# Performance work log

Measured on AMD Instinct MI355X. Metric: run time of the kernel, lower is better.

The kernel has to match this reference:

```python
import jax, jax.numpy as jnp
import numpy as np

B, S, H = 8, 2048, 256
MAX_SEQ = 2048


def get_rotary_matrix(context_window, embedding_dim):
    # Faithful to the llama-from-scratch construction (note the (i-1) quirk):
    # theta_i = 10000 ** (-2*(i-1)/d) for i in [0, d/2)
    half = embedding_dim // 2
    i = jnp.arange(half, dtype=jnp.float32)
    theta = jnp.power(10000.0, -2.0 * (i - 1.0) / embedding_dim)  # [half]
    pos = jnp.arange(context_window, dtype=jnp.float32)  # [S]
    ang = pos[:, None] * theta[None, :]  # [S, half]
    c, s = jnp.cos(ang), jnp.sin(ang)
    R = jnp.zeros((context_window, embedding_dim, embedding_dim), dtype=jnp.float32)
    idx = jnp.arange(half)
    R = R.at[:, 2 * idx, 2 * idx].set(c)
    R = R.at[:, 2 * idx, 2 * idx + 1].set(-s)
    R = R.at[:, 2 * idx + 1, 2 * idx].set(s)
    R = R.at[:, 2 * idx + 1, 2 * idx + 1].set(c)
    return R


def setup_inputs() -> dict:
    key = jax.random.key(0)
    kx, kq, kk, kv = jax.random.split(key, 4)
    scale = 1.0 / np.sqrt(H)
    x = jax.random.normal(kx, (B, S, H), dtype=jnp.float32)
    wq = jax.random.uniform(kq, (H, H), dtype=jnp.float32, minval=-scale, maxval=scale)
    wk = jax.random.uniform(kk, (H, H), dtype=jnp.float32, minval=-scale, maxval=scale)
    wv = jax.random.uniform(kv, (H, H), dtype=jnp.float32, minval=-scale, maxval=scale)
    r = get_rotary_matrix(MAX_SEQ, H)
    return {"x": x, "wq": wq, "wk": wk, "wv": wv, "r": r}


def reference(x, wq, wk, wv, r):
    b, s, h = x.shape
    # nn.Linear(bias=False): y = x @ W.T
    q = jnp.einsum("bsh,oh->bso", x, wq)
    k = jnp.einsum("bsh,oh->bso", x, wk)
    v = jnp.einsum("bsh,oh->bso", x, wv)
    # per-position dense rotary rotation: qr[b,s,:] = q[b,s,:] @ r[s]
    rs = r[:s]
    qr = jnp.einsum("bsh,shk->bsk", q, rs)
    kr = jnp.einsum("bsh,shk->bsk", k, rs)
    attn = jnp.einsum("bqh,bkh->bqk", qr, kr) * (h ** -0.5)  # [B,S,S]
    causal = jnp.tril(jnp.ones((s, s), dtype=bool))
    attn = jnp.where(causal[None, :, :], attn, -jnp.inf)
    attn = jax.nn.softmax(attn, axis=-1)
    out = jnp.einsum("bqk,bkh->bqh", attn, v)
    return out
```

## Files before the change

### kernel.cpp

```cpp
#include <hip/hip_runtime.h>


typedef __bf16 bf16x8 __attribute__((ext_vector_type(8)));
typedef float  f32x4  __attribute__((ext_vector_type(4)));
typedef unsigned short u16x4 __attribute__((ext_vector_type(4)));

#define LOG2E 1.44269504088896340736f
#define LOG2_10000 13.287712379549449f

__device__ __forceinline__ unsigned short f2bf(float f) {
    union { __bf16 h; unsigned short u; } cv;
    cv.h = (__bf16)f;
    return cv.u;
}

__device__ __forceinline__ void gl_lds16(const unsigned short* g, unsigned short* lds) {
    __builtin_amdgcn_global_load_lds(
        (const __attribute__((address_space(1))) unsigned int*)g,
        (__attribute__((address_space(3))) unsigned int*)lds, 16, 0, 0);
}

#define BARRIER_MEMFENCE() asm volatile("s_barrier" ::: "memory")
#define WAITVM(n) asm volatile("s_waitcnt vmcnt(" #n ")" ::: "memory")

__global__ __launch_bounds__(256) void prep(
    const float* __restrict__ wq, const float* __restrict__ wk,
    const float* __restrict__ wv,
    float2* __restrict__ cs, unsigned short* __restrict__ wb) {
    int bid = blockIdx.x;
    if (bid < 1024) {
        int id = bid * 256 + threadIdx.x;
        int s = id >> 7;
        int i = id & 127;
        float ex = -2.0f * ((float)i - 1.0f) * (1.0f / 256.0f);
        float theta = exp2f(LOG2_10000 * ex);
        float ang = (float)s * theta;
        float sn, c;
        sincosf(ang, &sn, &c);
        cs[id] = make_float2(c, sn);
    } else {
        int id = (bid - 1024) * 256 + threadIdx.x;
        int sel = id >> 14;
        int off = id & 16383;
        const float* src = (sel == 0) ? wq : (sel == 1) ? wk : wv;
        float4 d = ((const float4*)src)[off];
        u16x4 pk = { f2bf(d.x), f2bf(d.y), f2bf(d.z), f2bf(d.w) };
        *(u16x4*)&wb[(size_t)sel * 65536 + (size_t)off * 4] = pk;
    }
}

__global__ __launch_bounds__(256, 2) void qkv_rope(
    const float* __restrict__ x, const unsigned short* __restrict__ wb,
    const float2* __restrict__ cs,
    unsigned short* __restrict__ qr, unsigned short* __restrict__ kr,
    unsigned short* __restrict__ vt) {

    __shared__ unsigned short Ash[32 * 256];
    __shared__ unsigned short Bsh[256 * 128];

    const int mt  = blockIdx.x;
    const int tid = threadIdx.x;
    const int w = tid >> 6, l = tid & 63;
    const int lane_m = l & 15, quad = l >> 4;
    const int wm = w >> 1, wn = w & 1;

#pragma unroll
    for (int p = 0; p < 8; ++p) {
        int id = p * 256 + tid;
        int row = id >> 6, f4 = id & 63;
        float4 d = *(const float4*)(x + (size_t)(mt * 32 + row) * 256 + f4 * 4);
        u16x4 pk = { f2bf(d.x), f2bf(d.y), f2bf(d.z), f2bf(d.w) };
        int k = f4 * 4;
        int idx = row * 256 + ((((k >> 3) ^ row) << 3) | (k & 7));
        *(u16x4*)&Ash[idx] = pk;
    }

    for (int sel = 0; sel < 3; ++sel) {
        f32x4 acc[8];
#pragma unroll
        for (int c = 0; c < 8; ++c) acc[c] = (f32x4){0.f, 0.f, 0.f, 0.f};

        for (int kc2 = 0; kc2 < 2; ++kc2) {
            __syncthreads();
#pragma unroll
            for (int p = 0; p < 16; ++p) {
                int rb = (p * 4 + w) * 4;
                int rowg = rb + (l >> 4);
                int cg = (l & 15) ^ (rowg & 15);
                gl_lds16(wb + (size_t)sel * 65536 + (size_t)rowg * 256 + kc2 * 128 + cg * 8,
                         &Bsh[rb * 128]);
            }
            __syncthreads();
#pragma unroll
            for (int ks = 0; ks < 4; ++ks) {
                int ck = kc2 * 16 + ks * 4 + quad;
                int cl = ks * 4 + quad;
                int r0 = wm * 16 + lane_m;
                bf16x8 a0 = *(const bf16x8*)&Ash[r0 * 256 + ((ck ^ r0) << 3)];
#pragma unroll
                for (int ct = 0; ct < 8; ++ct) {
                    int nn = wn * 128 + ct * 16 + lane_m;
                    bf16x8 bb = *(const bf16x8*)&Bsh[nn * 128 + (((cl ^ (nn & 15))) << 3)];
                    acc[ct] = __builtin_amdgcn_mfma_f32_16x16x32_bf16(a0, bb, acc[ct], 0, 0, 0);
                }
            }
        }

        int mbase = mt * 32 + wm * 16 + quad * 4;
        if (sel < 2) {
            unsigned short* dst = sel ? kr : qr;
            const float scale = sel ? 1.0f : 0.0625f;
#pragma unroll
            for (int ct = 0; ct < 8; ++ct) {
                int col = wn * 128 + ct * 16 + lane_m;
                int ii = col >> 1;
                float sgn = (col & 1) ? -1.0f : 1.0f;
#pragma unroll
                for (int rr = 0; rr < 4; ++rr) {
                    int m = mbase + rr;
                    int spos = m & 2047;
                    float2 csv = cs[spos * 128 + ii];
                    float v = acc[ct][rr];
                    float pr = __shfl_xor(v, 1);
                    float rot = (csv.x * v + sgn * csv.y * pr) * scale;
                    dst[(size_t)m * 256 + col] = f2bf(rot);
                }
            }
        } else {
#pragma unroll
            for (int ct = 0; ct < 8; ++ct) {
                int col = wn * 128 + ct * 16 + lane_m;
                u16x4 pk = { f2bf(acc[ct][0]), f2bf(acc[ct][1]),
                             f2bf(acc[ct][2]), f2bf(acc[ct][3]) };
                int bb = mbase >> 11;
                int s0 = mbase & 2047;
                *(u16x4*)&vt[((size_t)bb * 256 + col) * 2048 + s0] = pk;
            }
        }
    }
}

__global__ __launch_bounds__(256, 2) void flash_attn(
    const unsigned short* __restrict__ qr, const unsigned short* __restrict__ kr,
    const unsigned short* __restrict__ vt, float* __restrict__ out) {

    __shared__ unsigned short Ksh[64 * 256];
    __shared__ unsigned short Vsh[256 * 64];
    __shared__ unsigned short Psh[32 * 64];

    const int n = blockIdx.x;
    const int b = n & 7;
    const int idx = n >> 3;
    const int j = (idx < 32) ? (63 - idx) : (idx - 32);
    const int q0 = j * 32;

    const int tid = threadIdx.x;
    const int w = tid >> 6, l = tid & 63;
    const int lane_m = l & 15, quad = l >> 4;

    bf16x8 qf[2][8];
    {
        const unsigned short* qb =
            qr + ((size_t)(b * 2048 + q0 + lane_m)) * 256 + quad * 8;
#pragma unroll
        for (int rt = 0; rt < 2; ++rt)
#pragma unroll
            for (int ks = 0; ks < 8; ++ks)
                qf[rt][ks] = *(const bf16x8*)(qb + rt * 16 * 256 + ks * 32);
    }

    const int nkt = ((q0 + 31) >> 6) + 1;

    auto stageK = [&](int kvbase) {
#pragma unroll
        for (int p = 0; p < 8; ++p) {
            int rb = (p * 4 + w) * 2;
            int row = rb + (l >> 5);
            int cg = (l & 31) ^ (row & 31);
            gl_lds16(kr + ((size_t)(b * 2048 + kvbase + row)) * 256 + cg * 8,
                     &Ksh[rb * 256]);
        }
    };
    auto stageV = [&](int kvbase) {
#pragma unroll
        for (int p = 0; p < 8; ++p) {
            int hb = (p * 4 + w) * 8;
            int h = hb + (l >> 3);
            int cg = (l & 7) ^ (h & 7);
            gl_lds16(vt + ((size_t)(b * 256 + h)) * 2048 + kvbase + cg * 8,
                     &Vsh[hb * 64]);
        }
    };

    stageK(0); stageV(0);
    WAITVM(0);
    BARRIER_MEMFENCE();

    f32x4 o[2][4];
#pragma unroll
    for (int rt = 0; rt < 2; ++rt)
#pragma unroll
        for (int ht = 0; ht < 4; ++ht) o[rt][ht] = (f32x4){0.f, 0.f, 0.f, 0.f};
    float l_loc[2][4] = {{0.f, 0.f, 0.f, 0.f}, {0.f, 0.f, 0.f, 0.f}};

    for (int t = 0; t < nkt; ++t) {
        const int kv0 = t * 64;
        const bool more = (t + 1) < nkt;

        f32x4 sacc[2];
        sacc[0] = (f32x4){0.f, 0.f, 0.f, 0.f};
        sacc[1] = (f32x4){0.f, 0.f, 0.f, 0.f};
        const int kvr = w * 16 + lane_m;
#pragma unroll
        for (int ks = 0; ks < 8; ++ks) {
            bf16x8 bb = *(const bf16x8*)
                &Ksh[kvr * 256 + (((ks * 4 + quad) ^ (kvr & 31)) << 3)];
            sacc[0] = __builtin_amdgcn_mfma_f32_16x16x32_bf16(qf[0][ks], bb, sacc[0], 0, 0, 0);
            sacc[1] = __builtin_amdgcn_mfma_f32_16x16x32_bf16(qf[1][ks], bb, sacc[1], 0, 0, 0);
        }
        BARRIER_MEMFENCE();

        if (more) stageK(kv0 + 64);

        const bool needmask = (kv0 + 63) > q0;
        const int colg = kv0 + w * 16 + lane_m;
#pragma unroll
        for (int rt = 0; rt < 2; ++rt) {
#pragma unroll
            for (int rr = 0; rr < 4; ++rr) {
                float e = exp2f(sacc[rt][rr] * LOG2E);
                if (needmask && colg > (q0 + rt * 16 + quad * 4 + rr)) e = 0.0f;
                l_loc[rt][rr] += e;
                int row = rt * 16 + quad * 4 + rr;
                int col = w * 16 + lane_m;
                Psh[row * 64 + ((((col >> 3) ^ (row & 7)) << 3) | (col & 7))] = f2bf(e);
            }
        }
        asm volatile("s_waitcnt lgkmcnt(0)" ::: "memory");
        if (more) { WAITVM(8); } else { WAITVM(0); }
        BARRIER_MEMFENCE();

#pragma unroll
        for (int ks2 = 0; ks2 < 2; ++ks2) {
            bf16x8 pa[2];
#pragma unroll
            for (int rt2 = 0; rt2 < 2; ++rt2) {
                int prow = rt2 * 16 + lane_m;
                pa[rt2] = *(const bf16x8*)
                    &Psh[prow * 64 + (((ks2 * 4 + quad) ^ (prow & 7)) << 3)];
            }
#pragma unroll
            for (int ht = 0; ht < 4; ++ht) {
                int h = w * 64 + ht * 16 + lane_m;
                bf16x8 vb = *(const bf16x8*)
                    &Vsh[h * 64 + (((ks2 * 4 + quad) ^ (h & 7)) << 3)];
                o[0][ht] = __builtin_amdgcn_mfma_f32_16x16x32_bf16(pa[0], vb, o[0][ht], 0, 0, 0);
                o[1][ht] = __builtin_amdgcn_mfma_f32_16x16x32_bf16(pa[1], vb, o[1][ht], 0, 0, 0);
            }
        }
        BARRIER_MEMFENCE();

        if (more) {
            stageV(kv0 + 64);
            WAITVM(8);
            BARRIER_MEMFENCE();
        }
    }

    __syncthreads();
    float* lbuf = (float*)Psh;
#pragma unroll
    for (int rt = 0; rt < 2; ++rt)
#pragma unroll
        for (int rr = 0; rr < 4; ++rr) {
            float v = l_loc[rt][rr];
            v += __shfl_xor(v, 1);
            v += __shfl_xor(v, 2);
            v += __shfl_xor(v, 4);
            v += __shfl_xor(v, 8);
            if (lane_m == 0) lbuf[w * 32 + rt * 16 + quad * 4 + rr] = v;
        }
    __syncthreads();
#pragma unroll
    for (int rt = 0; rt < 2; ++rt)
#pragma unroll
        for (int rr = 0; rr < 4; ++rr) {
            int row_l = rt * 16 + quad * 4 + rr;
            float inv = 1.0f / (lbuf[row_l] + lbuf[32 + row_l] +
                                lbuf[64 + row_l] + lbuf[96 + row_l]);
#pragma unroll
            for (int ht = 0; ht < 4; ++ht) {
                size_t idx2 = ((size_t)(b * 2048 + q0 + row_l)) * 256
                              + w * 64 + ht * 16 + lane_m;
                out[idx2] = o[rt][ht][rr] * inv;
            }
        }
}

extern "C" void kernel_launch(void* const* d_in, const int* in_sizes, int n_in,
                              void* d_out, int out_size, void* d_ws, size_t ws_size,
                              hipStream_t stream) {
    const float* x  = (const float*)d_in[0];
    const float* wq = (const float*)d_in[1];
    const float* wk = (const float*)d_in[2];
    const float* wv = (const float*)d_in[3];
    float* out = (float*)d_out;

    char* ws = (char*)d_ws;
    float2*         cs = (float2*)ws;
    unsigned short* qr = (unsigned short*)(ws + (2u << 20));
    unsigned short* kr = (unsigned short*)(ws + (10u << 20));
    unsigned short* vt = (unsigned short*)(ws + (18u << 20));
    unsigned short* wb = (unsigned short*)(ws + (26u << 20));

    prep<<<dim3(1216), dim3(256), 0, stream>>>(wq, wk, wv, cs, wb);
    qkv_rope<<<dim3(512), dim3(256), 0, stream>>>(x, wb, cs, qr, kr, vt);
    flash_attn<<<dim3(512), dim3(256), 0, stream>>>(qr, kr, vt, out);
    flash_attn<<<dim3(512), dim3(256), 0, stream>>>(qr, kr, vt, out);
}
```

Measured before the change: 704.1 us.

## Load K/V straight into registers, double-buffer P, drop duplicate attention launch

The attention kernel no longer stages K and V tiles through shared memory with async global-to-LDS copies. Each wave now loads only its own K rows and V columns directly into registers and prefetches the next tile while the current one is in use. P is double-buffered in LDS, so each iteration needs one barrier instead of several. The redundant second launch of flash_attn is also removed, cutting the attention work in half. In exchange, register pressure goes up, and each wave issues uncoalesced-ish strided global loads instead of sharing LDS tiles, so some of this data is fetched again by other blocks.

```diff
diff --git a/kernel.cpp b/kernel.cpp
--- a/kernel.cpp
+++ b/kernel.cpp
@@ -21,7 +21,6 @@
 }
 
 #define BARRIER_MEMFENCE() asm volatile("s_barrier" ::: "memory")
-#define WAITVM(n) asm volatile("s_waitcnt vmcnt(" #n ")" ::: "memory")
 
 __global__ __launch_bounds__(256) void prep(
     const float* __restrict__ wq, const float* __restrict__ wk,
@@ -144,9 +143,7 @@
     const unsigned short* __restrict__ qr, const unsigned short* __restrict__ kr,
     const unsigned short* __restrict__ vt, float* __restrict__ out) {
 
-    __shared__ unsigned short Ksh[64 * 256];
-    __shared__ unsigned short Vsh[256 * 64];
-    __shared__ unsigned short Psh[32 * 64];
+    __shared__ unsigned short Psh[2][32 * 64];
 
     const int n = blockIdx.x;
     const int b = n & 7;
@@ -171,30 +168,20 @@
 
     const int nkt = ((q0 + 31) >> 6) + 1;
 
-    auto stageK = [&](int kvbase) {
-#pragma unroll
-        for (int p = 0; p < 8; ++p) {
-            int rb = (p * 4 + w) * 2;
-            int row = rb + (l >> 5);
-            int cg = (l & 31) ^ (row & 31);
-            gl_lds16(kr + ((size_t)(b * 2048 + kvbase + row)) * 256 + cg * 8,
-                     &Ksh[rb * 256]);
-        }
-    };
-    auto stageV = [&](int kvbase) {
-#pragma unroll
-        for (int p = 0; p < 8; ++p) {
-            int hb = (p * 4 + w) * 8;
-            int h = hb + (l >> 3);
-            int cg = (l & 7) ^ (h & 7);
-            gl_lds16(vt + ((size_t)(b * 256 + h)) * 2048 + kvbase + cg * 8,
-                     &Vsh[hb * 64]);
-        }
-    };
-
-    stageK(0); stageV(0);
-    WAITVM(0);
-    BARRIER_MEMFENCE();
+    const unsigned short* kbase =
+        kr + ((size_t)(b * 2048 + w * 16 + lane_m)) * 256 + quad * 8;
+    const unsigned short* vbase =
+        vt + ((size_t)(b * 256 + w * 64 + lane_m)) * 2048 + quad * 8;
+
+    bf16x8 kf[8], vf[8];
+#pragma unroll
+    for (int ks = 0; ks < 8; ++ks)
+        kf[ks] = *(const bf16x8*)(kbase + ks * 32);
+#pragma unroll
+    for (int i = 0; i < 8; ++i) {
+        int ht = i & 3, ks2 = i >> 2;
+        vf[i] = *(const bf16x8*)(vbase + (size_t)ht * 16 * 2048 + ks2 * 32);
+    }
 
     f32x4 o[2][4];
 #pragma unroll
@@ -206,21 +193,23 @@
     for (int t = 0; t < nkt; ++t) {
         const int kv0 = t * 64;
         const bool more = (t + 1) < nkt;
+        unsigned short* P = &Psh[t & 1][0];
 
         f32x4 sacc[2];
         sacc[0] = (f32x4){0.f, 0.f, 0.f, 0.f};
         sacc[1] = (f32x4){0.f, 0.f, 0.f, 0.f};
-        const int kvr = w * 16 + lane_m;
 #pragma unroll
         for (int ks = 0; ks < 8; ++ks) {
-            bf16x8 bb = *(const bf16x8*)
-                &Ksh[kvr * 256 + (((ks * 4 + quad) ^ (kvr & 31)) << 3)];
-            sacc[0] = __builtin_amdgcn_mfma_f32_16x16x32_bf16(qf[0][ks], bb, sacc[0], 0, 0, 0);
-            sacc[1] = __builtin_amdgcn_mfma_f32_16x16x32_bf16(qf[1][ks], bb, sacc[1], 0, 0, 0);
-        }
-        BARRIER_MEMFENCE();
-
-        if (more) stageK(kv0 + 64);
+            sacc[0] = __builtin_amdgcn_mfma_f32_16x16x32_bf16(qf[0][ks], kf[ks], sacc[0], 0, 0, 0);
+            sacc[1] = __builtin_amdgcn_mfma_f32_16x16x32_bf16(qf[1][ks], kf[ks], sacc[1], 0, 0, 0);
+        }
+
+        if (more) {
+            const unsigned short* kb2 = kbase + (size_t)(kv0 + 64) * 256;
+#pragma unroll
+            for (int ks = 0; ks < 8; ++ks)
+                kf[ks] = *(const bf16x8*)(kb2 + ks * 32);
+        }
 
         const bool needmask = (kv0 + 63) > q0;
         const int colg = kv0 + w * 16 + lane_m;
@@ -233,11 +222,10 @@
                 l_loc[rt][rr] += e;
                 int row = rt * 16 + quad * 4 + rr;
                 int col = w * 16 + lane_m;
-                Psh[row * 64 + ((((col >> 3) ^ (row & 7)) << 3) | (col & 7))] = f2bf(e);
+                P[row * 64 + ((((col >> 3) ^ (row & 7)) << 3) | (col & 7))] = f2bf(e);
             }
         }
         asm volatile("s_waitcnt lgkmcnt(0)" ::: "memory");
-        if (more) { WAITVM(8); } else { WAITVM(0); }
         BARRIER_MEMFENCE();
 
 #pragma unroll
@@ -247,28 +235,27 @@
             for (int rt2 = 0; rt2 < 2; ++rt2) {
                 int prow = rt2 * 16 + lane_m;
                 pa[rt2] = *(const bf16x8*)
-                    &Psh[prow * 64 + (((ks2 * 4 + quad) ^ (prow & 7)) << 3)];
+                    &P[prow * 64 + (((ks2 * 4 + quad) ^ (prow & 7)) << 3)];
             }
 #pragma unroll
             for (int ht = 0; ht < 4; ++ht) {
-                int h = w * 64 + ht * 16 + lane_m;
-                bf16x8 vb = *(const bf16x8*)
-                    &Vsh[h * 64 + (((ks2 * 4 + quad) ^ (h & 7)) << 3)];
-                o[0][ht] = __builtin_amdgcn_mfma_f32_16x16x32_bf16(pa[0], vb, o[0][ht], 0, 0, 0);
-                o[1][ht] = __builtin_amdgcn_mfma_f32_16x16x32_bf16(pa[1], vb, o[1][ht], 0, 0, 0);
-            }
-        }
-        BARRIER_MEMFENCE();
+                o[0][ht] = __builtin_amdgcn_mfma_f32_16x16x32_bf16(pa[0], vf[ks2 * 4 + ht], o[0][ht], 0, 0, 0);
+                o[1][ht] = __builtin_amdgcn_mfma_f32_16x16x32_bf16(pa[1], vf[ks2 * 4 + ht], o[1][ht], 0, 0, 0);
+            }
+        }
 
         if (more) {
-            stageV(kv0 + 64);
-            WAITVM(8);
-            BARRIER_MEMFENCE();
+            const unsigned short* vb2 = vbase + (kv0 + 64);
+#pragma unroll
+            for (int i = 0; i < 8; ++i) {
+                int ht = i & 3, ks2 = i >> 2;
+                vf[i] = *(const bf16x8*)(vb2 + (size_t)ht * 16 * 2048 + ks2 * 32);
+            }
         }
     }
 
     __syncthreads();
-    float* lbuf = (float*)Psh;
+    float* lbuf = (float*)&Psh[0][0];
 #pragma unroll
     for (int rt = 0; rt < 2; ++rt)
 #pragma unroll
@@ -316,5 +303,4 @@
     prep<<<dim3(1216), dim3(256), 0, stream>>>(wq, wk, wv, cs, wb);
     qkv_rope<<<dim3(512), dim3(256), 0, stream>>>(x, wb, cs, qr, kr, vt);
     flash_attn<<<dim3(512), dim3(256), 0, stream>>>(qr, kr, vt, out);
-    flash_attn<<<dim3(512), dim3(256), 0, stream>>>(qr, kr, vt, out);
-}
+}
```

New measurement: 668.5 us. -5.1%, faster.

## Pair causal query tiles per block to share K/V staging; drop duplicate attention launch

Applied to the files above, without the earlier changes.

Each flash-attention block now runs 512 threads and handles two 32-row query tiles, a long one (63-p) and a short one (p). Both halves share the same K/V tiles staged in LDS, and each half has its own P buffer. Waves whose tile has already passed its causal range skip the compute but keep joining the barriers. The redundant second flash_attn launch is removed, which eliminates a full repeated pass of attention. The costs are higher register and LDS pressure per 512-thread block, and idle waves in the short half during later iterations.

```diff
diff --git a/kernel.cpp b/kernel.cpp
--- a/kernel.cpp
+++ b/kernel.cpp
@@ -140,23 +140,29 @@
     }
 }
 
-__global__ __launch_bounds__(256, 2) void flash_attn(
+__global__ __launch_bounds__(512, 2) void flash_attn(
     const unsigned short* __restrict__ qr, const unsigned short* __restrict__ kr,
     const unsigned short* __restrict__ vt, float* __restrict__ out) {
 
     __shared__ unsigned short Ksh[64 * 256];
     __shared__ unsigned short Vsh[256 * 64];
-    __shared__ unsigned short Psh[32 * 64];
+    __shared__ unsigned short Psh[2][32 * 64];
 
     const int n = blockIdx.x;
     const int b = n & 7;
-    const int idx = n >> 3;
-    const int j = (idx < 32) ? (63 - idx) : (idx - 32);
-    const int q0 = j * 32;
+    const int p = n >> 3;
+    const int q0a = (63 - p) * 32;
+    const int q0b = p * 32;
 
     const int tid = threadIdx.x;
     const int w = tid >> 6, l = tid & 63;
     const int lane_m = l & 15, quad = l >> 4;
+    const int qsel = w >> 2;
+    const int sub  = w & 3;
+
+    const int q0 = qsel ? q0b : q0a;
+    const int nktA = ((q0a + 31) >> 6) + 1;
+    const int nkt_my = ((q0 + 31) >> 6) + 1;
 
     bf16x8 qf[2][8];
     {
@@ -169,12 +175,10 @@
                 qf[rt][ks] = *(const bf16x8*)(qb + rt * 16 * 256 + ks * 32);
     }
 
-    const int nkt = ((q0 + 31) >> 6) + 1;
-
     auto stageK = [&](int kvbase) {
 #pragma unroll
-        for (int p = 0; p < 8; ++p) {
-            int rb = (p * 4 + w) * 2;
+        for (int pp = 0; pp < 4; ++pp) {
+            int rb = (pp * 8 + w) * 2;
             int row = rb + (l >> 5);
             int cg = (l & 31) ^ (row & 31);
             gl_lds16(kr + ((size_t)(b * 2048 + kvbase + row)) * 256 + cg * 8,
@@ -183,8 +187,8 @@
     };
     auto stageV = [&](int kvbase) {
 #pragma unroll
-        for (int p = 0; p < 8; ++p) {
-            int hb = (p * 4 + w) * 8;
+        for (int pp = 0; pp < 4; ++pp) {
+            int hb = (pp * 8 + w) * 8;
             int h = hb + (l >> 3);
             int cg = (l & 7) ^ (h & 7);
             gl_lds16(vt + ((size_t)(b * 256 + h)) * 2048 + kvbase + cg * 8,
@@ -203,72 +207,81 @@
         for (int ht = 0; ht < 4; ++ht) o[rt][ht] = (f32x4){0.f, 0.f, 0.f, 0.f};
     float l_loc[2][4] = {{0.f, 0.f, 0.f, 0.f}, {0.f, 0.f, 0.f, 0.f}};
 
-    for (int t = 0; t < nkt; ++t) {
+    unsigned short* P = &Psh[qsel][0];
+
+    for (int t = 0; t < nktA; ++t) {
         const int kv0 = t * 64;
-        const bool more = (t + 1) < nkt;
+        const bool more = (t + 1) < nktA;
+        const bool act = t < nkt_my;
 
         f32x4 sacc[2];
         sacc[0] = (f32x4){0.f, 0.f, 0.f, 0.f};
         sacc[1] = (f32x4){0.f, 0.f, 0.f, 0.f};
-        const int kvr = w * 16 + lane_m;
-#pragma unroll
-        for (int ks = 0; ks < 8; ++ks) {
-            bf16x8 bb = *(const bf16x8*)
-                &Ksh[kvr * 256 + (((ks * 4 + quad) ^ (kvr & 31)) << 3)];
-            sacc[0] = __builtin_amdgcn_mfma_f32_16x16x32_bf16(qf[0][ks], bb, sacc[0], 0, 0, 0);
-            sacc[1] = __builtin_amdgcn_mfma_f32_16x16x32_bf16(qf[1][ks], bb, sacc[1], 0, 0, 0);
+        if (act) {
+            const int kvr = sub * 16 + lane_m;
+#pragma unroll
+            for (int ks = 0; ks < 8; ++ks) {
+                bf16x8 bb = *(const bf16x8*)
+                    &Ksh[kvr * 256 + (((ks * 4 + quad) ^ (kvr & 31)) << 3)];
+                sacc[0] = __builtin_amdgcn_mfma_f32_16x16x32_bf16(qf[0][ks], bb, sacc[0], 0, 0, 0);
+                sacc[1] = __builtin_amdgcn_mfma_f32_16x16x32_bf16(qf[1][ks], bb, sacc[1], 0, 0, 0);
+            }
         }
         BARRIER_MEMFENCE();
 
         if (more) stageK(kv0 + 64);
 
-        const bool needmask = (kv0 + 63) > q0;
-        const int colg = kv0 + w * 16 + lane_m;
-#pragma unroll
-        for (int rt = 0; rt < 2; ++rt) {
-#pragma unroll
-            for (int rr = 0; rr < 4; ++rr) {
-                float e = exp2f(sacc[rt][rr] * LOG2E);
-                if (needmask && colg > (q0 + rt * 16 + quad * 4 + rr)) e = 0.0f;
-                l_loc[rt][rr] += e;
-                int row = rt * 16 + quad * 4 + rr;
-                int col = w * 16 + lane_m;
-                Psh[row * 64 + ((((col >> 3) ^ (row & 7)) << 3) | (col & 7))] = f2bf(e);
+        if (act) {
+            const bool needmask = (kv0 + 63) > q0;
+            const int colg = kv0 + sub * 16 + lane_m;
+#pragma unroll
+            for (int rt = 0; rt < 2; ++rt) {
+#pragma unroll
+                for (int rr = 0; rr < 4; ++rr) {
+                    float e = exp2f(sacc[rt][rr] * LOG2E);
+                    if (needmask && colg > (q0 + rt * 16 + quad * 4 + rr)) e = 0.0f;
+                    l_loc[rt][rr] += e;
+                    int row = rt * 16 + quad * 4 + rr;
+                    int col = sub * 16 + lane_m;
+                    P[row * 64 + ((((col >> 3) ^ (row & 7)) << 3) | (col & 7))] = f2bf(e);
+                }
             }
         }
         asm volatile("s_waitcnt lgkmcnt(0)" ::: "memory");
-        if (more) { WAITVM(8); } else { WAITVM(0); }
+        if (more) { WAITVM(4); } else { WAITVM(0); }
         BARRIER_MEMFENCE();
 
-#pragma unroll
-        for (int ks2 = 0; ks2 < 2; ++ks2) {
-            bf16x8 pa[2];
-#pragma unroll
-            for (int rt2 = 0; rt2 < 2; ++rt2) {
-                int prow = rt2 * 16 + lane_m;
-                pa[rt2] = *(const bf16x8*)
-                    &Psh[prow * 64 + (((ks2 * 4 + quad) ^ (prow & 7)) << 3)];
-            }
-#pragma unroll
-            for (int ht = 0; ht < 4; ++ht) {
-                int h = w * 64 + ht * 16 + lane_m;
-                bf16x8 vb = *(const bf16x8*)
-                    &Vsh[h * 64 + (((ks2 * 4 + quad) ^ (h & 7)) << 3)];
-                o[0][ht] = __builtin_amdgcn_mfma_f32_16x16x32_bf16(pa[0], vb, o[0][ht], 0, 0, 0);
-                o[1][ht] = __builtin_amdgcn_mfma_f32_16x16x32_bf16(pa[1], vb, o[1][ht], 0, 0, 0);
-            }
-        }
-        BARRIER_MEMFENCE();
+        if (act) {
+#pragma unroll
+            for (int ks2 = 0; ks2 < 2; ++ks2) {
+                bf16x8 pa[2];
+#pragma unroll
+                for (int rt2 = 0; rt2 < 2; ++rt2) {
+                    int prow = rt2 * 16 + lane_m;
+                    pa[rt2] = *(const bf16x8*)
+                        &P[prow * 64 + (((ks2 * 4 + quad) ^ (prow & 7)) << 3)];
+                }
+#pragma unroll
+                for (int ht = 0; ht < 4; ++ht) {
+                    int h = sub * 64 + ht * 16 + lane_m;
+                    bf16x8 vb = *(const bf16x8*)
+                        &Vsh[h * 64 + (((ks2 * 4 + quad) ^ (h & 7)) << 3)];
+                    o[0][ht] = __builtin_amdgcn_mfma_f32_16x16x32_bf16(pa[0], vb, o[0][ht], 0, 0, 0);
+                    o[1][ht] = __builtin_amdgcn_mfma_f32_16x16x32_bf16(pa[1], vb, o[1][ht], 0, 0, 0);
+                }
+            }
+        }
 
         if (more) {
+            BARRIER_MEMFENCE();
             stageV(kv0 + 64);
-            WAITVM(8);
+            WAITVM(4);
             BARRIER_MEMFENCE();
         }
     }
 
     __syncthreads();
-    float* lbuf = (float*)Psh;
+    float* lbuf = (float*)&Psh[0][0];
 #pragma unroll
     for (int rt = 0; rt < 2; ++rt)
 #pragma unroll
@@ -278,7 +291,8 @@
             v += __shfl_xor(v, 2);
             v += __shfl_xor(v, 4);
             v += __shfl_xor(v, 8);
-            if (lane_m == 0) lbuf[w * 32 + rt * 16 + quad * 4 + rr] = v;
+            if (lane_m == 0)
+                lbuf[(qsel * 4 + sub) * 32 + rt * 16 + quad * 4 + rr] = v;
         }
     __syncthreads();
 #pragma unroll
@@ -286,12 +300,12 @@
 #pragma unroll
         for (int rr = 0; rr < 4; ++rr) {
             int row_l = rt * 16 + quad * 4 + rr;
-            float inv = 1.0f / (lbuf[row_l] + lbuf[32 + row_l] +
-                                lbuf[64 + row_l] + lbuf[96 + row_l]);
+            const float* lb = &lbuf[qsel * 4 * 32 + row_l];
+            float inv = 1.0f / (lb[0] + lb[32] + lb[64] + lb[96]);
 #pragma unroll
             for (int ht = 0; ht < 4; ++ht) {
                 size_t idx2 = ((size_t)(b * 2048 + q0 + row_l)) * 256
-                              + w * 64 + ht * 16 + lane_m;
+                              + sub * 64 + ht * 16 + lane_m;
                 out[idx2] = o[rt][ht][rr] * inv;
             }
         }
@@ -315,6 +329,5 @@
 
     prep<<<dim3(1216), dim3(256), 0, stream>>>(wq, wk, wv, cs, wb);
     qkv_rope<<<dim3(512), dim3(256), 0, stream>>>(x, wb, cs, qr, kr, vt);
-    flash_attn<<<dim3(512), dim3(256), 0, stream>>>(qr, kr, vt, out);
-    flash_attn<<<dim3(512), dim3(256), 0, stream>>>(qr, kr, vt, out);
-}
+    flash_attn<<<dim3(256), dim3(512), 0, stream>>>(qr, kr, vt, out);
+}
```

New measurement: 651.1 us. 1.08x faster.
